# Performance work log

Hardware: AMD Instinct MI355X
Metric: run time of the kernel (lower is better)

## Reference

```python
import jax, jax.numpy as jnp
import numpy as np

L, N, E = 2048, 2, 1024
H = 16                      # num_heads
DH = E // H                 # head_dim = 64
SCALE = DH ** -0.5
NEG = -10000.0


def setup_inputs() -> dict:
    key = jax.random.key(0)
    ks = jax.random.split(key, 9)
    s = 0.02
    return {
        "query": jax.random.normal(ks[0], (L, N, E), jnp.float32),
        "q_proj": jax.random.normal(ks[1], (E, E), jnp.float32) * s,
        "q_bias": jax.random.normal(ks[2], (E,), jnp.float32) * s,
        "k_proj": jax.random.normal(ks[3], (E, E), jnp.float32) * s,
        "k_bias": jax.random.normal(ks[4], (E,), jnp.float32) * s,
        "v_proj": jax.random.normal(ks[5], (E, E), jnp.float32) * s,
        "v_bias": jax.random.normal(ks[6], (E,), jnp.float32) * s,
        "out_proj": jax.random.normal(ks[7], (E, E), jnp.float32) * s,
        "out_bias": jax.random.normal(ks[8], (E,), jnp.float32) * s,
    }


def reference(query, q_proj, q_bias, k_proj, k_bias, v_proj, v_bias, out_proj, out_bias):
    # query: [L, N, E]; projections act as F.linear: x @ W.T + b
    q = query @ q_proj.T + q_bias
    k = query @ k_proj.T + k_bias
    v = query @ v_proj.T + v_bias
    # [L, N*H, DH] -> [N*H, L, DH]
    q = q.reshape(L, N * H, DH).transpose(1, 0, 2) * SCALE
    k = k.reshape(L, N * H, DH).transpose(1, 0, 2)
    v = v.reshape(L, N * H, DH).transpose(1, 0, 2)
    attn = jnp.einsum('bqd,bkd->bqk', q, k)  # [N*H, L, L]
    causal = jnp.tril(jnp.ones((L, L), jnp.float32)) < 0.5  # True above diagonal
    attn = jnp.where(causal[None, :, :], NEG, attn)
    attn = jax.nn.softmax(attn, axis=-1)
    # dropout_p = 0.0 in training mode -> identity
    out = jnp.einsum('bqk,bkd->bqd', attn, v)  # [N*H, L, DH]
    out = out.transpose(1, 0, 2).reshape(L, N, H * DH)
    return out @ out_proj.T + out_bias
```

## Files before the change

### kernel.cpp

```cpp
#include <hip/hip_runtime.h>
#include <stdint.h>

typedef __attribute__((ext_vector_type(8)))  short          bf16x8;
typedef __attribute__((ext_vector_type(4)))  float          f32x4;
typedef __attribute__((ext_vector_type(16))) float          f32x16;
typedef __attribute__((ext_vector_type(4)))  unsigned int   u32x4;
typedef __attribute__((ext_vector_type(4)))  unsigned short u16x4;

#define SCALE_LOG2E 0.180336880f

static __device__ __forceinline__ unsigned short f2bf(float x) {
  union { float f; unsigned int u; } c; c.f = x;
  unsigned int r = c.u + 0x7fffu + ((c.u >> 16) & 1u);
  return (unsigned short)(r >> 16);
}

static __device__ __forceinline__ unsigned int cvt_pk_bf16(float lo, float hi) {
  unsigned int r;
  asm("v_cvt_pk_bf16_f32 %0, %1, %2" : "=v"(r) : "v"(lo), "v"(hi));
  return r;
}

static __device__ __forceinline__ void stage16(const unsigned short* g, unsigned short* l) {
  __builtin_amdgcn_global_load_lds(
      (const __attribute__((address_space(1))) unsigned int*)g,
      (__attribute__((address_space(3)))       unsigned int*)l, 16, 0, 0);
}

__global__ __launch_bounds__(256) void cvt_f32_bf16(const float* __restrict__ src,
                                                    unsigned short* __restrict__ dst, int n) {
  int i = (blockIdx.x * 256 + threadIdx.x) * 4;
  if (i < n) {
    float4 v = *(const float4*)(src + i);
    u16x4 o; o.x = f2bf(v.x); o.y = f2bf(v.y); o.z = f2bf(v.z); o.w = f2bf(v.w);
    *(u16x4*)(dst + i) = o;
  }
}

__global__ __launch_bounds__(256) void cvt_w4(const float* __restrict__ wq, const float* __restrict__ wk,
                                              const float* __restrict__ wv, const float* __restrict__ wo,
                                              unsigned short* __restrict__ dst) {
  const int z = blockIdx.y;
  const float* src = z == 0 ? wq : (z == 1 ? wk : (z == 2 ? wv : wo));
  int i = (blockIdx.x * 256 + threadIdx.x) * 4;
  float4 v = *(const float4*)(src + i);
  u16x4 o; o.x = f2bf(v.x); o.y = f2bf(v.y); o.z = f2bf(v.z); o.w = f2bf(v.w);
  *(u16x4*)(dst + (size_t)z * 1048576 + i) = o;
}

__device__ __forceinline__ void gemm_tile_core(const unsigned short* __restrict__ A,
                                               const unsigned short* __restrict__ B,
                                               int bi, int bj, f32x4 (&acc)[4][4]) {
  __shared__ unsigned short As[128 * 32];
  __shared__ unsigned short Bs[128 * 32];
  const int t = threadIdx.x, w = t >> 6, l = t & 63;
  const int l15 = l & 15, l4 = l >> 4;
  const int wm = w >> 1, wn = w & 1;
  const int srow = l >> 2;
  const int scol = ((l & 3) ^ ((l >> 3) & 3)) * 8;

#pragma unroll
  for (int m = 0; m < 4; m++)
#pragma unroll
    for (int n = 0; n < 4; n++)
#pragma unroll
      for (int r = 0; r < 4; r++) acc[m][n][r] = 0.f;

  const int koff = 8 * (l4 ^ ((l15 >> 1) & 3));
  for (int k0 = 0; k0 < 1024; k0 += 32) {
    stage16(A + (size_t)(bi * 128 + w * 16 + srow) * 1024 + k0 + scol, (unsigned short*)As + w * 512);
    stage16(A + (size_t)(bi * 128 + (w + 4) * 16 + srow) * 1024 + k0 + scol, (unsigned short*)As + (w + 4) * 512);
    stage16(B + (size_t)(bj * 128 + w * 16 + srow) * 1024 + k0 + scol, (unsigned short*)Bs + w * 512);
    stage16(B + (size_t)(bj * 128 + (w + 4) * 16 + srow) * 1024 + k0 + scol, (unsigned short*)Bs + (w + 4) * 512);
    __syncthreads();

    bf16x8 af[4], bfr[4];
#pragma unroll
    for (int m = 0; m < 4; m++) af[m]  = *(const bf16x8*)(As + (wm * 64 + m * 16 + l15) * 32 + koff);
#pragma unroll
    for (int n = 0; n < 4; n++) bfr[n] = *(const bf16x8*)(Bs + (wn * 64 + n * 16 + l15) * 32 + koff);
#pragma unroll
    for (int m = 0; m < 4; m++)
#pragma unroll
      for (int n = 0; n < 4; n++)
        acc[m][n] = __builtin_amdgcn_mfma_f32_16x16x32_bf16(af[m], bfr[n], acc[m][n], 0, 0, 0);
    __syncthreads();
  }
}

__global__ __launch_bounds__(256) void gemm_qkv(
    const unsigned short* __restrict__ X,
    const unsigned short* __restrict__ Wq, const unsigned short* __restrict__ Wk,
    const unsigned short* __restrict__ Wv,
    const float* __restrict__ bq, const float* __restrict__ bk, const float* __restrict__ bv,
    unsigned short* __restrict__ Qf, unsigned short* __restrict__ Kf, unsigned short* __restrict__ Vf) {
  const int mode = blockIdx.z;
  const unsigned short* W = mode == 0 ? Wq : (mode == 1 ? Wk : Wv);
  const float* bias = mode == 0 ? bq : (mode == 1 ? bk : bv);
  f32x4 acc[4][4];
  gemm_tile_core(X, W, blockIdx.y, blockIdx.x, acc);

  const int t = threadIdx.x, w = t >> 6, l = t & 63;
  const int l15 = l & 15, l4 = l >> 4;
  const int wm = w >> 1, wn = w & 1;
  const int i0 = blockIdx.y * 128 + wm * 64 + 4 * l4;
  const int j0 = blockIdx.x * 128 + wn * 64 + l15;
#pragma unroll
  for (int m = 0; m < 4; m++)
#pragma unroll
    for (int n = 0; n < 4; n++) {
      const int j = j0 + n * 16;
      const float bv_ = bias[j];
      const int h = j >> 6, d = j & 63;
#pragma unroll
      for (int r = 0; r < 4; r++) {
        const int i = i0 + m * 16 + r;
        const int n_ = i & 1, ll = i >> 1;
        const int b = n_ * 16 + h;
        const int kt = ll >> 5, l31k = ll & 31;
        float v = acc[m][n][r] + bv_;
        if (mode == 0) {
          const int lane = l31k + 32 * ((d >> 3) & 1);
          Qf[((size_t)(b * 64 + kt) * 4 + (d >> 4)) * 512 + lane * 8 + (d & 7)] = f2bf(v * SCALE_LOG2E);
        } else if (mode == 1) {
          const int lane = l31k + 32 * ((d >> 3) & 1);
          Kf[((size_t)(b * 64 + kt) * 4 + (d >> 4)) * 512 + lane * 8 + (d & 7)] = f2bf(v);
        } else {
          const int j2 = 2 * (d >> 5) + ((l31k >> 4) & 1);
          const int lane = (d & 31) + 32 * ((l31k >> 3) & 1);
          Vf[((size_t)(b * 64 + kt) * 4 + j2) * 512 + lane * 8 + (l31k & 7)] = f2bf(v);
        }
      }
    }
}

__global__ __launch_bounds__(256) void gemm_out(
    const unsigned short* __restrict__ X2, const unsigned short* __restrict__ Wo,
    const float* __restrict__ bias, float* __restrict__ out) {
  f32x4 acc[4][4];
  gemm_tile_core(X2, Wo, blockIdx.y, blockIdx.x, acc);
  const int t = threadIdx.x, w = t >> 6, l = t & 63;
  const int l15 = l & 15, l4 = l >> 4;
  const int wm = w >> 1, wn = w & 1;
  const int i0 = blockIdx.y * 128 + wm * 64 + 4 * l4;
  const int j0 = blockIdx.x * 128 + wn * 64 + l15;
#pragma unroll
  for (int m = 0; m < 4; m++)
#pragma unroll
    for (int n = 0; n < 4; n++) {
      const int j = j0 + n * 16;
      const float bv_ = bias[j];
#pragma unroll
      for (int r = 0; r < 4; r++)
        out[(size_t)(i0 + m * 16 + r) * 1024 + j] = acc[m][n][r] + bv_;
    }
}

static __device__ __forceinline__ void tile_step(
    const f32x16& sa, bool diag, int l31, int g,
    float& lsum, f32x16& o0, f32x16& o1, const bf16x8 (&vf)[4]) {
  float e[16];
#pragma unroll
  for (int r = 0; r < 16; r++) e[r] = sa[r];
  if (diag) {
#pragma unroll
    for (int r = 0; r < 16; r++) {
      const int kvloc = (r & 3) + 8 * (r >> 2) + 4 * g;
      e[r] = (kvloc <= l31) ? e[r] : -30000.f;
    }
  }
#pragma unroll
  for (int r = 0; r < 16; r++) e[r] = exp2f(e[r]);
  const float s0 = (e[0] + e[1]) + (e[2] + e[3]),   s1 = (e[4] + e[5]) + (e[6] + e[7]);
  const float s2 = (e[8] + e[9]) + (e[10] + e[11]), s3 = (e[12] + e[13]) + (e[14] + e[15]);
  lsum += (s0 + s1) + (s2 + s3);

  unsigned int u[8], pu[8];
#pragma unroll
  for (int i = 0; i < 8; i++) u[i] = cvt_pk_bf16(e[2 * i], e[2 * i + 1]);
#pragma unroll
  for (int i = 0; i < 8; i++) pu[i] = (unsigned int)__shfl_xor((int)u[i], 32, 64);
  u32x4 B0, B1;
  B0.x = g ? pu[2] : u[0];  B0.y = g ? pu[3] : u[1];
  B0.z = g ? u[2] : pu[0];  B0.w = g ? u[3] : pu[1];
  B1.x = g ? pu[6] : u[4];  B1.y = g ? pu[7] : u[5];
  B1.z = g ? u[6] : pu[4];  B1.w = g ? u[7] : pu[5];
  const bf16x8 pb0 = __builtin_bit_cast(bf16x8, B0);
  const bf16x8 pb1 = __builtin_bit_cast(bf16x8, B1);
  o0 = __builtin_amdgcn_mfma_f32_32x32x16_bf16(vf[0], pb0, o0, 0, 0, 0);
  o0 = __builtin_amdgcn_mfma_f32_32x32x16_bf16(vf[1], pb1, o0, 0, 0, 0);
  o1 = __builtin_amdgcn_mfma_f32_32x32x16_bf16(vf[2], pb0, o1, 0, 0, 0);
  o1 = __builtin_amdgcn_mfma_f32_32x32x16_bf16(vf[3], pb1, o1, 0, 0, 0);
}

__global__ __launch_bounds__(256, 2) void attn_kernel(
    const unsigned short* __restrict__ Qf, const unsigned short* __restrict__ Kf,
    const unsigned short* __restrict__ Vf, unsigned short* __restrict__ X2) {
  __shared__ float po[4 * 64 * 17];
  __shared__ float lb[2][4][32];

  const unsigned id = blockIdx.x;
  const int b = (id & 7) * 4 + ((id >> 3) & 3);
  const int p = id >> 5;
  const int t2 = 63 - p;

  const int w = threadIdx.x >> 6, l = threadIdx.x & 63;
  const int l31 = l & 31, g = l >> 5;

  const unsigned short* qp1 = Qf + ((size_t)(b * 64 + p) * 4) * 512 + l * 8;
  const unsigned short* qp2 = Qf + ((size_t)(b * 64 + t2) * 4) * 512 + l * 8;
  bf16x8 qf1[4], qf2[4];
#pragma unroll
  for (int s = 0; s < 4; s++) { qf1[s] = *(const bf16x8*)(qp1 + s * 512); qf2[s] = *(const bf16x8*)(qp2 + s * 512); }

  f32x16 z;
#pragma unroll
  for (int r = 0; r < 16; r++) z[r] = 0.f;
  f32x16 o10 = z, o11 = z, o20 = z, o21 = z;
  float ls1 = 0.f, ls2 = 0.f;

  const unsigned short* kb_ = Kf + (size_t)b * 131072;
  const unsigned short* vb_ = Vf + (size_t)b * 131072;

  bf16x8 kf[4], vf[4];
  {
    const unsigned short* kp = kb_ + w * 2048 + l * 8;
    const unsigned short* vp = vb_ + w * 2048 + l * 8;
#pragma unroll
    for (int s = 0; s < 4; s++) { kf[s] = *(const bf16x8*)(kp + s * 512); vf[s] = *(const bf16x8*)(vp + s * 512); }
  }

  for (int kt = w; kt <= t2; kt += 4) {
    const int ktn = (kt + 4 <= t2) ? kt + 4 : t2;
    const unsigned short* kp = kb_ + ktn * 2048 + l * 8;
    const unsigned short* vp = vb_ + ktn * 2048 + l * 8;
    bf16x8 kn[4], vn[4];
#pragma unroll
    for (int s = 0; s < 4; s++) { kn[s] = *(const bf16x8*)(kp + s * 512); vn[s] = *(const bf16x8*)(vp + s * 512); }
    __builtin_amdgcn_sched_barrier(0);

    f32x16 sa = __builtin_amdgcn_mfma_f32_32x32x16_bf16(kf[0], qf2[0], z, 0, 0, 0);
#pragma unroll
    for (int s = 1; s < 4; s++) sa = __builtin_amdgcn_mfma_f32_32x32x16_bf16(kf[s], qf2[s], sa, 0, 0, 0);
    tile_step(sa, kt == t2, l31, g, ls2, o20, o21, vf);

    if (kt <= p) {
      f32x16 sb = __builtin_amdgcn_mfma_f32_32x32x16_bf16(kf[0], qf1[0], z, 0, 0, 0);
#pragma unroll
      for (int s = 1; s < 4; s++) sb = __builtin_amdgcn_mfma_f32_32x32x16_bf16(kf[s], qf1[s], sb, 0, 0, 0);
      tile_step(sb, kt == p, l31, g, ls1, o10, o11, vf);
    }

#pragma unroll
    for (int s = 0; s < 4; s++) { kf[s] = kn[s]; vf[s] = vn[s]; }
  }

  const float ls1f = ls1 + __shfl_xor(ls1, 32, 64);
  const float ls2f = ls2 + __shfl_xor(ls2, 32, 64);
  float* mypo = po + (w * 64 + l) * 17;
  if (l < 32) { lb[0][w][l] = ls1f; lb[1][w][l] = ls2f; }
#pragma unroll
  for (int r = 0; r < 16; r++) mypo[r] = o10[r];
  __syncthreads();

  const float inv1 = 1.f / (lb[0][0][l31] + lb[0][1][l31] + lb[0][2][l31] + lb[0][3][l31]);
  const float inv2 = 1.f / (lb[1][0][l31] + lb[1][1][l31] + lb[1][2][l31] + lb[1][3][l31]);

  const int n_ = b >> 4, h = b & 15;
  unsigned short* orow1 = X2 + ((size_t)((32 * p + l31) * 2 + n_)) * 1024 + h * 64;
  unsigned short* orow2 = X2 + ((size_t)((32 * t2 + l31) * 2 + n_)) * 1024 + h * 64;
  const int dbase = 8 * w + 4 * g;
  float c[4];

#pragma unroll
  for (int j = 0; j < 4; j++) c[j] = 0.f;
#pragma unroll
  for (int s = 0; s < 4; s++) {
    const float* pp = po + (s * 64 + l) * 17 + w * 4;
#pragma unroll
    for (int j = 0; j < 4; j++) c[j] += pp[j];
  }
#pragma unroll
  for (int j = 0; j < 4; j++) orow1[dbase + j] = f2bf(c[j] * inv1);
  __syncthreads();

#pragma unroll
  for (int r = 0; r < 16; r++) mypo[r] = o11[r];
  __syncthreads();
#pragma unroll
  for (int j = 0; j < 4; j++) c[j] = 0.f;
#pragma unroll
  for (int s = 0; s < 4; s++) {
    const float* pp = po + (s * 64 + l) * 17 + w * 4;
#pragma unroll
    for (int j = 0; j < 4; j++) c[j] += pp[j];
  }
#pragma unroll
  for (int j = 0; j < 4; j++) orow1[32 + dbase + j] = f2bf(c[j] * inv1);
  __syncthreads();

#pragma unroll
  for (int r = 0; r < 16; r++) mypo[r] = o20[r];
  __syncthreads();
#pragma unroll
  for (int j = 0; j < 4; j++) c[j] = 0.f;
#pragma unroll
  for (int s = 0; s < 4; s++) {
    const float* pp = po + (s * 64 + l) * 17 + w * 4;
#pragma unroll
    for (int j = 0; j < 4; j++) c[j] += pp[j];
  }
#pragma unroll
  for (int j = 0; j < 4; j++) orow2[dbase + j] = f2bf(c[j] * inv2);
  __syncthreads();

#pragma unroll
  for (int r = 0; r < 16; r++) mypo[r] = o21[r];
  __syncthreads();
#pragma unroll
  for (int j = 0; j < 4; j++) c[j] = 0.f;
#pragma unroll
  for (int s = 0; s < 4; s++) {
    const float* pp = po + (s * 64 + l) * 17 + w * 4;
#pragma unroll
    for (int j = 0; j < 4; j++) c[j] += pp[j];
  }
#pragma unroll
  for (int j = 0; j < 4; j++) orow2[32 + dbase + j] = f2bf(c[j] * inv2);
}

extern "C" void kernel_launch(void* const* d_in, const int* in_sizes, int n_in,
                              void* d_out, int out_size, void* d_ws, size_t ws_size,
                              hipStream_t stream) {
  const float* query    = (const float*)d_in[0];
  const float* q_proj   = (const float*)d_in[1];
  const float* q_bias   = (const float*)d_in[2];
  const float* k_proj   = (const float*)d_in[3];
  const float* k_bias   = (const float*)d_in[4];
  const float* v_proj   = (const float*)d_in[5];
  const float* v_bias   = (const float*)d_in[6];
  const float* out_proj = (const float*)d_in[7];
  const float* out_bias = (const float*)d_in[8];
  float* out = (float*)d_out;

  char* ws = (char*)d_ws;
  unsigned short* Xq = (unsigned short*)(ws);
  unsigned short* Wq = (unsigned short*)(ws + (8u << 20));
  unsigned short* Qf = (unsigned short*)(ws + (16u << 20));
  unsigned short* Kf = (unsigned short*)(ws + (24u << 20));
  unsigned short* Vf = (unsigned short*)(ws + (32u << 20));
  unsigned short* X2 = (unsigned short*)(ws + (40u << 20));
  unsigned short* Wk = Wq + 1048576;
  unsigned short* Wv = Wq + 2097152;
  unsigned short* Wo = Wq + 3145728;

  cvt_f32_bf16<<<4096, 256, 0, stream>>>(query, Xq, 4194304);
  cvt_w4<<<dim3(1024, 4), 256, 0, stream>>>(q_proj, k_proj, v_proj, out_proj, Wq);

  gemm_qkv<<<dim3(8, 32, 3), 256, 0, stream>>>(Xq, Wq, Wk, Wv, q_bias, k_bias, v_bias, Qf, Kf, Vf);
  attn_kernel<<<1024, 256, 0, stream>>>(Qf, Kf, Vf, X2);
  gemm_out<<<dim3(8, 32), 256, 0, stream>>>(X2, Wo, out_bias, out);
}
```

Measured before the change: 108.8 us.

## Prefetch K/V tiles via global_load_lds into per-wave LDS staging

Replaces the register double-buffered K/V prefetch with asynchronous global-to-LDS loads into a per-wave staging buffer. Each iteration waits for the staged tile, reads it into registers, then issues the next tile's load before the MFMA work. Removing the extra kn/vn registers frees VGPRs, and the launch bounds are raised from 2 to 3 blocks per SIMD to allow more waves in flight. The cost is 32KB of extra LDS per block, which may itself cap occupancy, plus an extra LDS read per tile and a full vmcnt wait at the top of each iteration.

```diff
diff --git a/kernel.cpp b/kernel.cpp
--- a/kernel.cpp
+++ b/kernel.cpp
@@ -193,9 +193,10 @@
   o1 = __builtin_amdgcn_mfma_f32_32x32x16_bf16(vf[3], pb1, o1, 0, 0, 0);
 }
 
-__global__ __launch_bounds__(256, 2) void attn_kernel(
+__global__ __launch_bounds__(256, 3) void attn_kernel(
     const unsigned short* __restrict__ Qf, const unsigned short* __restrict__ Kf,
     const unsigned short* __restrict__ Vf, unsigned short* __restrict__ X2) {
+  __shared__ unsigned short stg[4][4096];
   __shared__ float po[4 * 64 * 17];
   __shared__ float lb[2][4][32];
 
@@ -206,6 +207,7 @@
 
   const int w = threadIdx.x >> 6, l = threadIdx.x & 63;
   const int l31 = l & 31, g = l >> 5;
+  unsigned short* ws_ = stg[w];
 
   const unsigned short* qp1 = Qf + ((size_t)(b * 64 + p) * 4) * 512 + l * 8;
   const unsigned short* qp2 = Qf + ((size_t)(b * 64 + t2) * 4) * 512 + l * 8;
@@ -213,31 +215,46 @@
 #pragma unroll
   for (int s = 0; s < 4; s++) { qf1[s] = *(const bf16x8*)(qp1 + s * 512); qf2[s] = *(const bf16x8*)(qp2 + s * 512); }
 
+  const unsigned short* kb_ = Kf + (size_t)b * 131072;
+  const unsigned short* vb_ = Vf + (size_t)b * 131072;
+
+  {
+    const unsigned short* kp = kb_ + w * 2048;
+    const unsigned short* vp = vb_ + w * 2048;
+#pragma unroll
+    for (int c = 0; c < 4; c++) {
+      stage16(kp + c * 512 + l * 8, ws_ + c * 512);
+      stage16(vp + c * 512 + l * 8, ws_ + 2048 + c * 512);
+    }
+  }
+
   f32x16 z;
 #pragma unroll
   for (int r = 0; r < 16; r++) z[r] = 0.f;
   f32x16 o10 = z, o11 = z, o20 = z, o21 = z;
   float ls1 = 0.f, ls2 = 0.f;
 
-  const unsigned short* kb_ = Kf + (size_t)b * 131072;
-  const unsigned short* vb_ = Vf + (size_t)b * 131072;
-
-  bf16x8 kf[4], vf[4];
-  {
-    const unsigned short* kp = kb_ + w * 2048 + l * 8;
-    const unsigned short* vp = vb_ + w * 2048 + l * 8;
-#pragma unroll
-    for (int s = 0; s < 4; s++) { kf[s] = *(const bf16x8*)(kp + s * 512); vf[s] = *(const bf16x8*)(vp + s * 512); }
-  }
-
   for (int kt = w; kt <= t2; kt += 4) {
-    const int ktn = (kt + 4 <= t2) ? kt + 4 : t2;
-    const unsigned short* kp = kb_ + ktn * 2048 + l * 8;
-    const unsigned short* vp = vb_ + ktn * 2048 + l * 8;
-    bf16x8 kn[4], vn[4];
-#pragma unroll
-    for (int s = 0; s < 4; s++) { kn[s] = *(const bf16x8*)(kp + s * 512); vn[s] = *(const bf16x8*)(vp + s * 512); }
+    asm volatile("s_waitcnt vmcnt(0)" ::: "memory");
     __builtin_amdgcn_sched_barrier(0);
+    bf16x8 kf[4], vf[4];
+#pragma unroll
+    for (int s = 0; s < 4; s++) {
+      kf[s] = *(const bf16x8*)(ws_ + s * 512 + l * 8);
+      vf[s] = *(const bf16x8*)(ws_ + 2048 + s * 512 + l * 8);
+    }
+    asm volatile("s_waitcnt lgkmcnt(0)" ::: "memory");
+    __builtin_amdgcn_sched_barrier(0);
+    {
+      const int ktn = (kt + 4 <= t2) ? kt + 4 : t2;
+      const unsigned short* kp = kb_ + ktn * 2048;
+      const unsigned short* vp = vb_ + ktn * 2048;
+#pragma unroll
+      for (int c = 0; c < 4; c++) {
+        stage16(kp + c * 512 + l * 8, ws_ + c * 512);
+        stage16(vp + c * 512 + l * 8, ws_ + 2048 + c * 512);
+      }
+    }
 
     f32x16 sa = __builtin_amdgcn_mfma_f32_32x32x16_bf16(kf[0], qf2[0], z, 0, 0, 0);
 #pragma unroll
@@ -250,10 +267,8 @@
       for (int s = 1; s < 4; s++) sb = __builtin_amdgcn_mfma_f32_32x32x16_bf16(kf[s], qf1[s], sb, 0, 0, 0);
       tile_step(sb, kt == p, l31, g, ls1, o10, o11, vf);
     }
-
-#pragma unroll
-    for (int s = 0; s < 4; s++) { kf[s] = kn[s]; vf[s] = vn[s]; }
-  }
+  }
+  asm volatile("s_waitcnt vmcnt(0)" ::: "memory");
 
   const float ls1f = ls1 + __shfl_xor(ls1, 32, 64);
   const float ls2f = ls2 + __shfl_xor(ls2, 32, 64);
```

New measurement: 116.7 us. 7.3% more time.
